# Kernel tuning notes

Measured on AMD Instinct MI355X. Metric: run time of the kernel, lower is better.

## Reference

```python
import jax, jax.numpy as jnp
import numpy as np

B, S, C, H = 8, 8192, 512, 128


def setup_inputs() -> dict:
    key = jax.random.key(0)
    k1, k2 = jax.random.split(key)
    x = jax.random.normal(k1, (B, S, C), dtype=jnp.float32)
    # nn.Linear default init: U(-1/sqrt(fan_in), 1/sqrt(fan_in))
    bound = 1.0 / np.sqrt(C)
    W = jax.random.uniform(k2, (C, H), dtype=jnp.float32, minval=-bound, maxval=bound)
    b = jnp.zeros((H,), dtype=jnp.float32)
    return {"x": x, "W": W, "b": b}


def reference(x, W, b):
    # block = identity; attn = Linear(C->H) then Softmax over sequence dim (dim=1)
    logits = jnp.einsum("bsc,ch->bsh", x, W) + b          # [B, S, H]
    a = jax.nn.softmax(logits, axis=1)                     # softmax over S
    ctx = jnp.einsum("bsh,bsc->bhc", a, x)                 # a^T @ x  -> [B, H, C]
    return jnp.einsum("bsh,bhc->bsc", a, ctx)              # a @ (a^T @ x)
```

## Files before the change

### kernel.cpp

```cpp
#include <hip/hip_runtime.h>

typedef float  f32x4 __attribute__((ext_vector_type(4)));
typedef short  s16x8 __attribute__((ext_vector_type(8)));
typedef unsigned short u16;

#define OFF_E     0ULL
#define OFF_ET    16777216ULL
#define OFF_EPART 33554432ULL
#define OFF_GT    67108864ULL
#define OFF_WT    68157440ULL
#define OFF_ZP    68288512ULL
#define OFF_RZ2   68550656ULL
#define WS_NEED   68554752ULL

#define GLL16(g, l)                                                          \
  __builtin_amdgcn_global_load_lds(                                          \
      (const __attribute__((address_space(1))) void*)(g),                    \
      (__attribute__((address_space(3))) void*)(l), 16, 0, 0)

#define KEY3(r) ((((r) >> 3) ^ ((r) << 1)) & 7)

__device__ __forceinline__ u16 f2bf(float f) {
  unsigned u = __float_as_uint(f);
  return (u16)((u + 0x8000u) >> 16);
}
__device__ __forceinline__ unsigned pack2(float a, float b) {
  unsigned ua = __float_as_uint(a), ub = __float_as_uint(b);
  return ((ua + 0x8000u) >> 16) | ((ub + 0x8000u) & 0xffff0000u);
}

__global__ __launch_bounds__(256) void k_wt(const float* __restrict__ W,
                                            u16* __restrict__ WtImg) {
  int idx = blockIdx.x * 256 + threadIdx.x;
  int h = idx & 127, c = idx >> 7;
  int kt = c >> 6, oct = (c >> 3) & 7, t = c & 7;
  WtImg[kt * 8192 + h * 64 + ((oct ^ (h & 7)) * 8) + t] = f2bf(W[c * 128 + h]);
}

__global__ __launch_bounds__(256) void k_logits_e(
    const float* __restrict__ x, const u16* __restrict__ WtImg,
    u16* __restrict__ eImg, u16* __restrict__ eTImg, float* __restrict__ zpart) {
  __shared__ __align__(16) u16 smem[4 * 8192];
  __shared__ float zs[512];
  u16* const sm = smem;
  const int tid = threadIdx.x;
  const int lane = tid & 63, wave = tid >> 6;
  const int l15 = lane & 15, quad = lane >> 4;
  const int mt = blockIdx.x;
  const int rowBase = mt << 7;
  const int q = tid & 3, rb = tid >> 2;

  f32x4 acc[2][8];
#pragma unroll
  for (int i = 0; i < 2; ++i)
#pragma unroll
    for (int j = 0; j < 8; ++j) acc[i][j] = (f32x4){0.f, 0.f, 0.f, 0.f};

  f32x4 xv[2][4];

  {
    const char* srcB = (const char*)WtImg + wave * 4096 + lane * 16;
    char* dstB = (char*)(smem + 16384) + wave * 4096;
#pragma unroll
    for (int i = 0; i < 4; ++i) GLL16(srcB + i * 1024, dstB + i * 1024);
  }
#pragma unroll
  for (int rep = 0; rep < 2; ++rep) {
    const int r = rb + rep * 64;
    const float* src = x + (size_t)(rowBase + r) * 512 + q * 4;
#pragma unroll
    for (int j = 0; j < 4; ++j) xv[rep][j] = *(const f32x4*)(src + j * 16);
  }
#pragma unroll
  for (int rep = 0; rep < 2; ++rep) {
    const int r = rb + rep * 64;
#pragma unroll
    for (int j = 0; j < 4; ++j) {
      const int chunk = (2 * j + (q >> 1)) ^ (r & 7);
      unsigned* dst = (unsigned*)&smem[r * 64 + chunk * 8 + (q & 1) * 4];
      dst[0] = pack2(xv[rep][j][0], xv[rep][j][1]);
      dst[1] = pack2(xv[rep][j][2], xv[rep][j][3]);
    }
  }
  __syncthreads();

  for (int kt = 0; kt < 8; ++kt) {
    const int cur = kt & 1;
    u16* lAc = smem + (cur ? 8192 : 0);
    u16* lBc = smem + 16384 + (cur ? 8192 : 0);
    if (kt < 7) {
      const char* srcB = (const char*)WtImg + (size_t)(kt + 1) * 16384 + wave * 4096 + lane * 16;
      char* dstB = (char*)(smem + 16384 + (cur ? 0 : 8192)) + wave * 4096;
#pragma unroll
      for (int i = 0; i < 4; ++i) GLL16(srcB + i * 1024, dstB + i * 1024);
      const int k0 = (kt + 1) << 6;
#pragma unroll
      for (int rep = 0; rep < 2; ++rep) {
        const int r = rb + rep * 64;
        const float* src = x + (size_t)(rowBase + r) * 512 + k0 + q * 4;
#pragma unroll
        for (int j = 0; j < 4; ++j) xv[rep][j] = *(const f32x4*)(src + j * 16);
      }
    }
#pragma unroll
    for (int kk = 0; kk < 2; ++kk) {
      s16x8 af[2], bf[8];
#pragma unroll
      for (int i = 0; i < 2; ++i) {
        const int r = wave * 32 + i * 16 + l15;
        af[i] = *(const s16x8*)&lAc[r * 64 + (((kk * 4 + quad) ^ (r & 7)) * 8)];
      }
#pragma unroll
      for (int j = 0; j < 8; ++j) {
        const int r = j * 16 + l15;
        bf[j] = *(const s16x8*)&lBc[r * 64 + (((kk * 4 + quad) ^ (r & 7)) * 8)];
      }
#pragma unroll
      for (int i = 0; i < 2; ++i)
#pragma unroll
        for (int j = 0; j < 8; ++j)
          acc[i][j] = __builtin_amdgcn_mfma_f32_16x16x32_bf16(af[i], bf[j], acc[i][j], 0, 0, 0);
    }
    if (kt < 7) {
      u16* lAn = smem + (cur ? 0 : 8192);
#pragma unroll
      for (int rep = 0; rep < 2; ++rep) {
        const int r = rb + rep * 64;
#pragma unroll
        for (int j = 0; j < 4; ++j) {
          const int chunk = (2 * j + (q >> 1)) ^ (r & 7);
          unsigned* dst = (unsigned*)&lAn[r * 64 + chunk * 8 + (q & 1) * 4];
          dst[0] = pack2(xv[rep][j][0], xv[rep][j][1]);
          dst[1] = pack2(xv[rep][j][2], xv[rep][j][3]);
        }
      }
    }
    __syncthreads();
  }

  float ex[2][8][4];
  float cs[8];
#pragma unroll
  for (int j = 0; j < 8; ++j) cs[j] = 0.f;
#pragma unroll
  for (int i = 0; i < 2; ++i)
#pragma unroll
    for (int j = 0; j < 8; ++j)
#pragma unroll
      for (int rr = 0; rr < 4; ++rr) {
        float l = acc[i][j][rr];
        l = fminf(fmaxf(l, -30.f), 30.f);
        float t = __expf(l);
        ex[i][j][rr] = t;
        cs[j] += t;
      }
#pragma unroll
  for (int j = 0; j < 8; ++j) {
    cs[j] += __shfl_xor(cs[j], 16);
    cs[j] += __shfl_xor(cs[j], 32);
  }
  if (quad == 0) {
#pragma unroll
    for (int j = 0; j < 8; ++j) zs[wave * 128 + j * 16 + l15] = cs[j];
  }
  __syncthreads();

#pragma unroll
  for (int i = 0; i < 2; ++i)
#pragma unroll
    for (int j = 0; j < 8; ++j)
#pragma unroll
      for (int rr = 0; rr < 4; ++rr) {
        int s = wave * 32 + i * 16 + quad * 4 + rr;
        int h = j * 16 + l15;
        sm[s * 128 + (((h >> 3) ^ (s & 15)) * 8) + (h & 7)] = f2bf(ex[i][j][rr]);
      }
  if (tid < 128)
    zpart[mt * 128 + tid] = zs[tid] + zs[128 + tid] + zs[256 + tid] + zs[384 + tid];
  __syncthreads();

  {
    char* dstT = (char*)eImg + (size_t)mt * 32768;
    const char* smB = (const char*)sm;
#pragma unroll
    for (int pass = 0; pass < 8; ++pass) {
      s16x8 v = *(const s16x8*)(smB + pass * 4096 + tid * 16);
      *(s16x8*)(dstT + pass * 4096 + tid * 16) = v;
    }
  }
  {
    int ck = tid & 15, hb = tid >> 4;
    int cH = ck >> 3, oct = ck & 7;
    u16* dstT = eTImg + (size_t)mt * 16384 + cH * 8192;
#pragma unroll
    for (int pass = 0; pass < 8; ++pass) {
      int h = hb + pass * 16;
      s16x8 v;
#pragma unroll
      for (int j = 0; j < 8; ++j) {
        int s = ck * 8 + j;
        v[j] = (short)sm[s * 128 + (((h >> 3) ^ (s & 15)) * 8) + (h & 7)];
      }
      *(s16x8*)(dstT + h * 64 + ((oct ^ KEY3(h)) * 8)) = v;
    }
  }
}

__global__ __launch_bounds__(256) void k_E(const float* __restrict__ x,
                                           const u16* __restrict__ eTImg,
                                           float* __restrict__ Epart) {
  __shared__ __align__(16) u16 smem[4 * 8192];
  const int tid = threadIdx.x;
  const int lane = tid & 63, wave = tid >> 6;
  const int l15 = lane & 15, quad = lane >> 4;
  const int nt = blockIdx.x;
  const int b = blockIdx.y;
  const int kc = blockIdx.z;
  const int cw = tid & 15, rg = tid >> 4;

  f32x4 acc[2][8];
#pragma unroll
  for (int i = 0; i < 2; ++i)
#pragma unroll
    for (int j = 0; j < 8; ++j) acc[i][j] = (f32x4){0.f, 0.f, 0.f, 0.f};

  f32x4 xv[4][2];

  {
    const char* srcB = (const char*)eTImg + ((size_t)(b * 128 + kc * 8) * 16384) +
                       wave * 4096 + lane * 16;
    char* dstB = (char*)(smem + 16384) + wave * 4096;
#pragma unroll
    for (int i = 0; i < 4; ++i) GLL16(srcB + i * 1024, dstB + i * 1024);
  }
  {
    const float* src = x + ((size_t)(b * 8192 + kc * 512 + rg * 4) * 512 + nt * 128 + cw * 8);
#pragma unroll
    for (int j = 0; j < 4; ++j) {
      xv[j][0] = *(const f32x4*)(src + (size_t)j * 512);
      xv[j][1] = *(const f32x4*)(src + (size_t)j * 512 + 4);
    }
  }
#pragma unroll
  for (int i = 0; i < 8; ++i) {
    const int cl = cw * 8 + i;
    unsigned wv[2];
    if (i < 4) {
      wv[0] = pack2(xv[0][0][i], xv[1][0][i]);
      wv[1] = pack2(xv[2][0][i], xv[3][0][i]);
    } else {
      wv[0] = pack2(xv[0][1][i - 4], xv[1][1][i - 4]);
      wv[1] = pack2(xv[2][1][i - 4], xv[3][1][i - 4]);
    }
    *(unsigned*)&smem[cl * 64 + (((rg >> 1) ^ KEY3(cl)) * 8) + (rg & 1) * 4] = wv[0];
    *(unsigned*)&smem[cl * 64 + (((rg >> 1) ^ KEY3(cl)) * 8) + (rg & 1) * 4 + 2] = wv[1];
  }
  __syncthreads();

  for (int kt = 0; kt < 8; ++kt) {
    const int cur = kt & 1;
    u16* lAc = smem + (cur ? 8192 : 0);
    u16* lBc = smem + 16384 + (cur ? 8192 : 0);
    if (kt < 7) {
      const char* srcB = (const char*)eTImg +
                         ((size_t)(b * 128 + kc * 8 + kt + 1) * 16384) +
                         wave * 4096 + lane * 16;
      char* dstB = (char*)(smem + 16384 + (cur ? 0 : 8192)) + wave * 4096;
#pragma unroll
      for (int i = 0; i < 4; ++i) GLL16(srcB + i * 1024, dstB + i * 1024);
      const float* src = x + ((size_t)(b * 8192 + kc * 512 + (kt + 1) * 64 + rg * 4) * 512 +
                              nt * 128 + cw * 8);
#pragma unroll
      for (int j = 0; j < 4; ++j) {
        xv[j][0] = *(const f32x4*)(src + (size_t)j * 512);
        xv[j][1] = *(const f32x4*)(src + (size_t)j * 512 + 4);
      }
    }
#pragma unroll
    for (int kk = 0; kk < 2; ++kk) {
      s16x8 af[2], bf[8];
#pragma unroll
      for (int i = 0; i < 2; ++i) {
        const int r = wave * 32 + i * 16 + l15;
        af[i] = *(const s16x8*)&lAc[r * 64 + (((kk * 4 + quad) ^ KEY3(r)) * 8)];
      }
#pragma unroll
      for (int j = 0; j < 8; ++j) {
        const int n = j * 16 + l15;
        bf[j] = *(const s16x8*)&lBc[n * 64 + (((kk * 4 + quad) ^ KEY3(n)) * 8)];
      }
#pragma unroll
      for (int i = 0; i < 2; ++i)
#pragma unroll
        for (int j = 0; j < 8; ++j)
          acc[i][j] = __builtin_amdgcn_mfma_f32_16x16x32_bf16(af[i], bf[j], acc[i][j], 0, 0, 0);
    }
    if (kt < 7) {
      u16* lAn = smem + (cur ? 0 : 8192);
#pragma unroll
      for (int i = 0; i < 8; ++i) {
        const int cl = cw * 8 + i;
        unsigned wv[2];
        if (i < 4) {
          wv[0] = pack2(xv[0][0][i], xv[1][0][i]);
          wv[1] = pack2(xv[2][0][i], xv[3][0][i]);
        } else {
          wv[0] = pack2(xv[0][1][i - 4], xv[1][1][i - 4]);
          wv[1] = pack2(xv[2][1][i - 4], xv[3][1][i - 4]);
        }
        *(unsigned*)&lAn[cl * 64 + (((rg >> 1) ^ KEY3(cl)) * 8) + (rg & 1) * 4] = wv[0];
        *(unsigned*)&lAn[cl * 64 + (((rg >> 1) ^ KEY3(cl)) * 8) + (rg & 1) * 4 + 2] = wv[1];
      }
    }
    __syncthreads();
  }
  float* dst = Epart + ((size_t)(kc * 8 + b) * 512 + nt * 128) * 128;
#pragma unroll
  for (int i = 0; i < 2; ++i)
#pragma unroll
    for (int j = 0; j < 8; ++j)
#pragma unroll
      for (int rr = 0; rr < 4; ++rr) {
        int c = wave * 32 + i * 16 + quad * 4 + rr;
        int h = j * 16 + l15;
        dst[(size_t)c * 128 + h] = acc[i][j][rr];
      }
}

__global__ __launch_bounds__(256) void k_G(const float* __restrict__ Epart,
                                           const float* __restrict__ zpart,
                                           u16* __restrict__ GtImg) {
  __shared__ float rzs[128];
  const int tid = threadIdx.x;
  const int bidx = blockIdx.x;
  const int b = bidx >> 5;
  if (tid < 128) {
    float z = 0.f;
#pragma unroll 8
    for (int i = 0; i < 64; ++i) z += zpart[(b * 64 + i) * 128 + tid];
    rzs[tid] = 1.0f / (z * z);
  }
  __syncthreads();
  int idx = bidx * 256 + tid;
  int h8 = idx & 15, c = (idx >> 4) & 511;
  f32x4 s0 = {0.f, 0.f, 0.f, 0.f}, s1 = {0.f, 0.f, 0.f, 0.f};
#pragma unroll
  for (int p = 0; p < 16; ++p) {
    const float* src = Epart + (((size_t)(p * 8 + b) * 512 + c) * 128 + h8 * 8);
    s0 += *(const f32x4*)src;
    s1 += *(const f32x4*)(src + 4);
  }
  f32x4 z0 = *(const f32x4*)&rzs[h8 * 8];
  f32x4 z1 = *(const f32x4*)&rzs[h8 * 8 + 4];
  unsigned ov[4];
  ov[0] = pack2(s0[0] * z0[0], s0[1] * z0[1]);
  ov[1] = pack2(s0[2] * z0[2], s0[3] * z0[3]);
  ov[2] = pack2(s1[0] * z1[0], s1[1] * z1[1]);
  ov[3] = pack2(s1[2] * z1[2], s1[3] * z1[3]);
  int r = c & 63, ct = c >> 6;
  *(s16x8*)(GtImg + ((size_t)(b * 8 + ct) * 8192) + r * 128 + ((h8 ^ (r & 15)) * 8)) =
      *(s16x8*)ov;
}

__global__ __launch_bounds__(256) void k_out(const u16* __restrict__ eImg,
                                             const u16* __restrict__ GtImg,
                                             float* __restrict__ out) {
  __shared__ __align__(16) u16 lA[128 * 128];
  __shared__ __align__(16) u16 lBd[2 * 64 * 128];
  const int tid = threadIdx.x;
  const int lane = tid & 63, wave = tid >> 6;
  const int l15 = lane & 15, quad = lane >> 4;
  const int st = blockIdx.x;
  const int b = blockIdx.y;

  {
    const char* src = (const char*)eImg + ((size_t)(b * 64 + st) * 32768) +
                      wave * 8192 + lane * 16;
    char* dst = (char*)lA + wave * 8192;
#pragma unroll
    for (int i = 0; i < 8; ++i) GLL16(src + i * 1024, dst + i * 1024);
  }
  {
    const char* src = (const char*)GtImg + ((size_t)(b * 8) * 16384) +
                      wave * 4096 + lane * 16;
    char* dst = (char*)lBd + wave * 4096;
#pragma unroll
    for (int i = 0; i < 4; ++i) GLL16(src + i * 1024, dst + i * 1024);
  }
  __syncthreads();

  for (int ct = 0; ct < 8; ++ct) {
    const int cur = ct & 1;
    u16* lBc = lBd + (cur ? 8192 : 0);
    if (ct < 7) {
      const char* src = (const char*)GtImg + ((size_t)(b * 8 + ct + 1) * 16384) +
                        wave * 4096 + lane * 16;
      char* dst = (char*)(lBd + (cur ? 0 : 8192)) + wave * 4096;
#pragma unroll
      for (int i = 0; i < 4; ++i) GLL16(src + i * 1024, dst + i * 1024);
    }
    f32x4 acc[2][4];
#pragma unroll
    for (int i = 0; i < 2; ++i)
#pragma unroll
      for (int j = 0; j < 4; ++j) acc[i][j] = (f32x4){0.f, 0.f, 0.f, 0.f};
#pragma unroll
    for (int kk = 0; kk < 4; ++kk) {
      s16x8 af[2], bf[4];
#pragma unroll
      for (int i = 0; i < 2; ++i) {
        const int r = wave * 32 + i * 16 + l15;
        af[i] = *(const s16x8*)&lA[r * 128 + (((kk * 4 + quad) ^ (r & 15)) * 8)];
      }
#pragma unroll
      for (int j = 0; j < 4; ++j) {
        const int n = j * 16 + l15;
        bf[j] = *(const s16x8*)&lBc[n * 128 + (((kk * 4 + quad) ^ (n & 15)) * 8)];
      }
#pragma unroll
      for (int i = 0; i < 2; ++i)
#pragma unroll
        for (int j = 0; j < 4; ++j)
          acc[i][j] = __builtin_amdgcn_mfma_f32_16x16x32_bf16(af[i], bf[j], acc[i][j], 0, 0, 0);
    }
#pragma unroll
    for (int i = 0; i < 2; ++i)
#pragma unroll
      for (int j = 0; j < 4; ++j)
#pragma unroll
        for (int rr = 0; rr < 4; ++rr) {
          int s = wave * 32 + i * 16 + quad * 4 + rr;
          int c = ct * 64 + j * 16 + l15;
          __builtin_nontemporal_store(
              acc[i][j][rr], &out[(size_t)(b * 8192 + st * 128 + s) * 512 + c]);
        }
    __syncthreads();
  }
}

extern "C" void kernel_launch(void* const* d_in, const int* in_sizes, int n_in,
                              void* d_out, int out_size, void* d_ws, size_t ws_size,
                              hipStream_t stream) {
  if (ws_size < (size_t)WS_NEED) return;
  const float* x = (const float*)d_in[0];
  const float* W = (const float*)d_in[1];
  float* out = (float*)d_out;
  char* ws = (char*)d_ws;
  u16* eImg = (u16*)(ws + OFF_E);
  u16* eTImg = (u16*)(ws + OFF_ET);
  float* Epart = (float*)(ws + OFF_EPART);
  u16* GtImg = (u16*)(ws + OFF_GT);
  u16* WtImg = (u16*)(ws + OFF_WT);
  float* zpart = (float*)(ws + OFF_ZP);

  k_wt<<<256, 256, 0, stream>>>(W, WtImg);
  k_logits_e<<<512, 256, 0, stream>>>(x, WtImg, eImg, eTImg, zpart);
  k_E<<<dim3(4, 8, 16), 256, 0, stream>>>(x, eTImg, Epart);
  k_G<<<256, 256, 0, stream>>>(Epart, zpart, GtImg);
  k_out<<<dim3(64, 8), 256, 0, stream>>>(eImg, GtImg, out);
}
```

Before: 301.7 us.

## Fuse five kernel launches into one persistent kernel with grid barriers

Merges the weight transpose, logits/exp, E partial GEMM, G reduction and output GEMM into a single 512-block kernel, with atomic-counter grid barriers between phases. The goal is to remove the launch gaps and tail idle time between the five separate kernels. This relies on all 512 blocks being co-resident (launch_bounds 256,2 with about 66KB of shared memory per block). The spin barriers add their own cost, and the phases keep the same block counts as before.

```diff
diff --git a/kernel.cpp b/kernel.cpp
--- a/kernel.cpp
+++ b/kernel.cpp
@@ -10,8 +10,10 @@
 #define OFF_GT    67108864ULL
 #define OFF_WT    68157440ULL
 #define OFF_ZP    68288512ULL
-#define OFF_RZ2   68550656ULL
+#define OFF_BAR   68550656ULL
 #define WS_NEED   68554752ULL
+
+#define NBLK 512u
 
 #define GLL16(g, l)                                                          \
   __builtin_amdgcn_global_load_lds(                                          \
@@ -29,247 +31,229 @@
   return ((ua + 0x8000u) >> 16) | ((ub + 0x8000u) & 0xffff0000u);
 }
 
-__global__ __launch_bounds__(256) void k_wt(const float* __restrict__ W,
-                                            u16* __restrict__ WtImg) {
-  int idx = blockIdx.x * 256 + threadIdx.x;
-  int h = idx & 127, c = idx >> 7;
-  int kt = c >> 6, oct = (c >> 3) & 7, t = c & 7;
-  WtImg[kt * 8192 + h * 64 + ((oct ^ (h & 7)) * 8) + t] = f2bf(W[c * 128 + h]);
-}
-
-__global__ __launch_bounds__(256) void k_logits_e(
-    const float* __restrict__ x, const u16* __restrict__ WtImg,
-    u16* __restrict__ eImg, u16* __restrict__ eTImg, float* __restrict__ zpart) {
-  __shared__ __align__(16) u16 smem[4 * 8192];
-  __shared__ float zs[512];
-  u16* const sm = smem;
+__device__ __forceinline__ void gbar(unsigned* cnt) {
+  __syncthreads();
+  if (threadIdx.x == 0) {
+    __threadfence();
+    atomicAdd(cnt, 1u);
+    while (atomicAdd(cnt, 0u) < NBLK) __builtin_amdgcn_s_sleep(2);
+    __threadfence();
+  }
+  __syncthreads();
+}
+
+__global__ void k_init(unsigned* bar) {
+  if (threadIdx.x < 8) bar[threadIdx.x] = 0u;
+}
+
+__global__ __launch_bounds__(256, 2) void k_fused(
+    const float* __restrict__ x, const float* __restrict__ W,
+    float* __restrict__ out, u16* __restrict__ eImg, u16* __restrict__ eTImg,
+    float* __restrict__ Epart, u16* __restrict__ GtImg, u16* __restrict__ WtImg,
+    float* __restrict__ zpart, unsigned* bar) {
+  __shared__ __align__(16) char SMEM[67584];
   const int tid = threadIdx.x;
+  const int bid = blockIdx.x;
   const int lane = tid & 63, wave = tid >> 6;
   const int l15 = lane & 15, quad = lane >> 4;
-  const int mt = blockIdx.x;
-  const int rowBase = mt << 7;
-  const int q = tid & 3, rb = tid >> 2;
-
-  f32x4 acc[2][8];
-#pragma unroll
-  for (int i = 0; i < 2; ++i)
-#pragma unroll
-    for (int j = 0; j < 8; ++j) acc[i][j] = (f32x4){0.f, 0.f, 0.f, 0.f};
-
-  f32x4 xv[2][4];
+
+  if (tid < 128) {
+    int idx = bid * 128 + tid;
+    int h = idx & 127, c = idx >> 7;
+    int kt = c >> 6, oct = (c >> 3) & 7, t = c & 7;
+    WtImg[kt * 8192 + h * 64 + ((oct ^ (h & 7)) * 8) + t] = f2bf(W[c * 128 + h]);
+  }
+  gbar(bar + 0);
 
   {
-    const char* srcB = (const char*)WtImg + wave * 4096 + lane * 16;
-    char* dstB = (char*)(smem + 16384) + wave * 4096;
-#pragma unroll
-    for (int i = 0; i < 4; ++i) GLL16(srcB + i * 1024, dstB + i * 1024);
-  }
-#pragma unroll
-  for (int rep = 0; rep < 2; ++rep) {
-    const int r = rb + rep * 64;
-    const float* src = x + (size_t)(rowBase + r) * 512 + q * 4;
-#pragma unroll
-    for (int j = 0; j < 4; ++j) xv[rep][j] = *(const f32x4*)(src + j * 16);
-  }
-#pragma unroll
-  for (int rep = 0; rep < 2; ++rep) {
-    const int r = rb + rep * 64;
-#pragma unroll
-    for (int j = 0; j < 4; ++j) {
-      const int chunk = (2 * j + (q >> 1)) ^ (r & 7);
-      unsigned* dst = (unsigned*)&smem[r * 64 + chunk * 8 + (q & 1) * 4];
-      dst[0] = pack2(xv[rep][j][0], xv[rep][j][1]);
-      dst[1] = pack2(xv[rep][j][2], xv[rep][j][3]);
-    }
-  }
-  __syncthreads();
-
-  for (int kt = 0; kt < 8; ++kt) {
-    const int cur = kt & 1;
-    u16* lAc = smem + (cur ? 8192 : 0);
-    u16* lBc = smem + 16384 + (cur ? 8192 : 0);
-    if (kt < 7) {
-      const char* srcB = (const char*)WtImg + (size_t)(kt + 1) * 16384 + wave * 4096 + lane * 16;
-      char* dstB = (char*)(smem + 16384 + (cur ? 0 : 8192)) + wave * 4096;
+    u16* smem = (u16*)SMEM;
+    float* zs = (float*)(SMEM + 65536);
+    u16* const sm = smem;
+    const int mt = bid;
+    const int rowBase = mt << 7;
+    const int q = tid & 3, rb = tid >> 2;
+
+    f32x4 acc[2][8];
+#pragma unroll
+    for (int i = 0; i < 2; ++i)
+#pragma unroll
+      for (int j = 0; j < 8; ++j) acc[i][j] = (f32x4){0.f, 0.f, 0.f, 0.f};
+
+    f32x4 xv[2][4];
+
+    {
+      const char* srcB = (const char*)WtImg + wave * 4096 + lane * 16;
+      char* dstB = (char*)(smem + 16384) + wave * 4096;
 #pragma unroll
       for (int i = 0; i < 4; ++i) GLL16(srcB + i * 1024, dstB + i * 1024);
-      const int k0 = (kt + 1) << 6;
-#pragma unroll
-      for (int rep = 0; rep < 2; ++rep) {
-        const int r = rb + rep * 64;
-        const float* src = x + (size_t)(rowBase + r) * 512 + k0 + q * 4;
-#pragma unroll
-        for (int j = 0; j < 4; ++j) xv[rep][j] = *(const f32x4*)(src + j * 16);
-      }
-    }
-#pragma unroll
-    for (int kk = 0; kk < 2; ++kk) {
-      s16x8 af[2], bf[8];
-#pragma unroll
-      for (int i = 0; i < 2; ++i) {
-        const int r = wave * 32 + i * 16 + l15;
-        af[i] = *(const s16x8*)&lAc[r * 64 + (((kk * 4 + quad) ^ (r & 7)) * 8)];
-      }
-#pragma unroll
-      for (int j = 0; j < 8; ++j) {
-        const int r = j * 16 + l15;
-        bf[j] = *(const s16x8*)&lBc[r * 64 + (((kk * 4 + quad) ^ (r & 7)) * 8)];
-      }
-#pragma unroll
-      for (int i = 0; i < 2; ++i)
-#pragma unroll
-        for (int j = 0; j < 8; ++j)
-          acc[i][j] = __builtin_amdgcn_mfma_f32_16x16x32_bf16(af[i], bf[j], acc[i][j], 0, 0, 0);
-    }
-    if (kt < 7) {
-      u16* lAn = smem + (cur ? 0 : 8192);
-#pragma unroll
-      for (int rep = 0; rep < 2; ++rep) {
-        const int r = rb + rep * 64;
-#pragma unroll
-        for (int j = 0; j < 4; ++j) {
-          const int chunk = (2 * j + (q >> 1)) ^ (r & 7);
-          unsigned* dst = (unsigned*)&lAn[r * 64 + chunk * 8 + (q & 1) * 4];
-          dst[0] = pack2(xv[rep][j][0], xv[rep][j][1]);
-          dst[1] = pack2(xv[rep][j][2], xv[rep][j][3]);
-        }
-      }
-    }
-    __syncthreads();
-  }
-
-  float ex[2][8][4];
-  float cs[8];
-#pragma unroll
-  for (int j = 0; j < 8; ++j) cs[j] = 0.f;
-#pragma unroll
-  for (int i = 0; i < 2; ++i)
-#pragma unroll
-    for (int j = 0; j < 8; ++j)
-#pragma unroll
-      for (int rr = 0; rr < 4; ++rr) {
-        float l = acc[i][j][rr];
-        l = fminf(fmaxf(l, -30.f), 30.f);
-        float t = __expf(l);
-        ex[i][j][rr] = t;
-        cs[j] += t;
-      }
-#pragma unroll
-  for (int j = 0; j < 8; ++j) {
-    cs[j] += __shfl_xor(cs[j], 16);
-    cs[j] += __shfl_xor(cs[j], 32);
-  }
-  if (quad == 0) {
-#pragma unroll
-    for (int j = 0; j < 8; ++j) zs[wave * 128 + j * 16 + l15] = cs[j];
-  }
-  __syncthreads();
-
-#pragma unroll
-  for (int i = 0; i < 2; ++i)
-#pragma unroll
-    for (int j = 0; j < 8; ++j)
-#pragma unroll
-      for (int rr = 0; rr < 4; ++rr) {
-        int s = wave * 32 + i * 16 + quad * 4 + rr;
-        int h = j * 16 + l15;
-        sm[s * 128 + (((h >> 3) ^ (s & 15)) * 8) + (h & 7)] = f2bf(ex[i][j][rr]);
-      }
-  if (tid < 128)
-    zpart[mt * 128 + tid] = zs[tid] + zs[128 + tid] + zs[256 + tid] + zs[384 + tid];
-  __syncthreads();
+    }
+#pragma unroll
+    for (int rep = 0; rep < 2; ++rep) {
+      const int r = rb + rep * 64;
+      const float* src = x + (size_t)(rowBase + r) * 512 + q * 4;
+#pragma unroll
+      for (int j = 0; j < 4; ++j) xv[rep][j] = *(const f32x4*)(src + j * 16);
+    }
+#pragma unroll
+    for (int rep = 0; rep < 2; ++rep) {
+      const int r = rb + rep * 64;
+#pragma unroll
+      for (int j = 0; j < 4; ++j) {
+        const int chunk = (2 * j + (q >> 1)) ^ (r & 7);
+        unsigned* dst = (unsigned*)&smem[r * 64 + chunk * 8 + (q & 1) * 4];
+        dst[0] = pack2(xv[rep][j][0], xv[rep][j][1]);
+        dst[1] = pack2(xv[rep][j][2], xv[rep][j][3]);
+      }
+    }
+    __syncthreads();
+
+    for (int kt = 0; kt < 8; ++kt) {
+      const int cur = kt & 1;
+      u16* lAc = smem + (cur ? 8192 : 0);
+      u16* lBc = smem + 16384 + (cur ? 8192 : 0);
+      if (kt < 7) {
+        const char* srcB = (const char*)WtImg + (size_t)(kt + 1) * 16384 + wave * 4096 + lane * 16;
+        char* dstB = (char*)(smem + 16384 + (cur ? 0 : 8192)) + wave * 4096;
+#pragma unroll
+        for (int i = 0; i < 4; ++i) GLL16(srcB + i * 1024, dstB + i * 1024);
+        const int k0 = (kt + 1) << 6;
+#pragma unroll
+        for (int rep = 0; rep < 2; ++rep) {
+          const int r = rb + rep * 64;
+          const float* src = x + (size_t)(rowBase + r) * 512 + k0 + q * 4;
+#pragma unroll
+          for (int j = 0; j < 4; ++j) xv[rep][j] = *(const f32x4*)(src + j * 16);
+        }
+      }
+#pragma unroll
+      for (int kk = 0; kk < 2; ++kk) {
+        s16x8 af[2], bf[8];
+#pragma unroll
+        for (int i = 0; i < 2; ++i) {
+          const int r = wave * 32 + i * 16 + l15;
+          af[i] = *(const s16x8*)&lAc[r * 64 + (((kk * 4 + quad) ^ (r & 7)) * 8)];
+        }
+#pragma unroll
+        for (int j = 0; j < 8; ++j) {
+          const int r = j * 16 + l15;
+          bf[j] = *(const s16x8*)&lBc[r * 64 + (((kk * 4 + quad) ^ (r & 7)) * 8)];
+        }
+#pragma unroll
+        for (int i = 0; i < 2; ++i)
+#pragma unroll
+          for (int j = 0; j < 8; ++j)
+            acc[i][j] = __builtin_amdgcn_mfma_f32_16x16x32_bf16(af[i], bf[j], acc[i][j], 0, 0, 0);
+      }
+      if (kt < 7) {
+        u16* lAn = smem + (cur ? 0 : 8192);
+#pragma unroll
+        for (int rep = 0; rep < 2; ++rep) {
+          const int r = rb + rep * 64;
+#pragma unroll
+          for (int j = 0; j < 4; ++j) {
+            const int chunk = (2 * j + (q >> 1)) ^ (r & 7);
+            unsigned* dst = (unsigned*)&lAn[r * 64 + chunk * 8 + (q & 1) * 4];
+            dst[0] = pack2(xv[rep][j][0], xv[rep][j][1]);
+            dst[1] = pack2(xv[rep][j][2], xv[rep][j][3]);
+          }
+        }
+      }
+      __syncthreads();
+    }
+
+    float ex[2][8][4];
+    float cs[8];
+#pragma unroll
+    for (int j = 0; j < 8; ++j) cs[j] = 0.f;
+#pragma unroll
+    for (int i = 0; i < 2; ++i)
+#pragma unroll
+      for (int j = 0; j < 8; ++j)
+#pragma unroll
+        for (int rr = 0; rr < 4; ++rr) {
+          float l = acc[i][j][rr];
+          l = fminf(fmaxf(l, -30.f), 30.f);
+          float t = __expf(l);
+          ex[i][j][rr] = t;
+          cs[j] += t;
+        }
+#pragma unroll
+    for (int j = 0; j < 8; ++j) {
+      cs[j] += __shfl_xor(cs[j], 16);
+      cs[j] += __shfl_xor(cs[j], 32);
+    }
+    if (quad == 0) {
+#pragma unroll
+      for (int j = 0; j < 8; ++j) zs[wave * 128 + j * 16 + l15] = cs[j];
+    }
+    __syncthreads();
+
+#pragma unroll
+    for (int i = 0; i < 2; ++i)
+#pragma unroll
+      for (int j = 0; j < 8; ++j)
+#pragma unroll
+        for (int rr = 0; rr < 4; ++rr) {
+          int s = wave * 32 + i * 16 + quad * 4 + rr;
+          int h = j * 16 + l15;
+          sm[s * 128 + (((h >> 3) ^ (s & 15)) * 8) + (h & 7)] = f2bf(ex[i][j][rr]);
+        }
+    if (tid < 128)
+      zpart[mt * 128 + tid] = zs[tid] + zs[128 + tid] + zs[256 + tid] + zs[384 + tid];
+    __syncthreads();
+
+    {
+      char* dstT = (char*)eImg + (size_t)mt * 32768;
+      const char* smB = (const char*)sm;
+#pragma unroll
+      for (int pass = 0; pass < 8; ++pass) {
+        s16x8 v = *(const s16x8*)(smB + pass * 4096 + tid * 16);
+        *(s16x8*)(dstT + pass * 4096 + tid * 16) = v;
+      }
+    }
+    {
+      int ck = tid & 15, hb = tid >> 4;
+      int cH = ck >> 3, oct = ck & 7;
+      u16* dstT = eTImg + (size_t)mt * 16384 + cH * 8192;
+#pragma unroll
+      for (int pass = 0; pass < 8; ++pass) {
+        int h = hb + pass * 16;
+        s16x8 v;
+#pragma unroll
+        for (int j = 0; j < 8; ++j) {
+          int s = ck * 8 + j;
+          v[j] = (short)sm[s * 128 + (((h >> 3) ^ (s & 15)) * 8) + (h & 7)];
+        }
+        *(s16x8*)(dstT + h * 64 + ((oct ^ KEY3(h)) * 8)) = v;
+      }
+    }
+  }
+  gbar(bar + 1);
 
   {
-    char* dstT = (char*)eImg + (size_t)mt * 32768;
-    const char* smB = (const char*)sm;
-#pragma unroll
-    for (int pass = 0; pass < 8; ++pass) {
-      s16x8 v = *(const s16x8*)(smB + pass * 4096 + tid * 16);
-      *(s16x8*)(dstT + pass * 4096 + tid * 16) = v;
-    }
-  }
-  {
-    int ck = tid & 15, hb = tid >> 4;
-    int cH = ck >> 3, oct = ck & 7;
-    u16* dstT = eTImg + (size_t)mt * 16384 + cH * 8192;
-#pragma unroll
-    for (int pass = 0; pass < 8; ++pass) {
-      int h = hb + pass * 16;
-      s16x8 v;
-#pragma unroll
-      for (int j = 0; j < 8; ++j) {
-        int s = ck * 8 + j;
-        v[j] = (short)sm[s * 128 + (((h >> 3) ^ (s & 15)) * 8) + (h & 7)];
-      }
-      *(s16x8*)(dstT + h * 64 + ((oct ^ KEY3(h)) * 8)) = v;
-    }
-  }
-}
-
-__global__ __launch_bounds__(256) void k_E(const float* __restrict__ x,
-                                           const u16* __restrict__ eTImg,
-                                           float* __restrict__ Epart) {
-  __shared__ __align__(16) u16 smem[4 * 8192];
-  const int tid = threadIdx.x;
-  const int lane = tid & 63, wave = tid >> 6;
-  const int l15 = lane & 15, quad = lane >> 4;
-  const int nt = blockIdx.x;
-  const int b = blockIdx.y;
-  const int kc = blockIdx.z;
-  const int cw = tid & 15, rg = tid >> 4;
-
-  f32x4 acc[2][8];
-#pragma unroll
-  for (int i = 0; i < 2; ++i)
-#pragma unroll
-    for (int j = 0; j < 8; ++j) acc[i][j] = (f32x4){0.f, 0.f, 0.f, 0.f};
-
-  f32x4 xv[4][2];
-
-  {
-    const char* srcB = (const char*)eTImg + ((size_t)(b * 128 + kc * 8) * 16384) +
-                       wave * 4096 + lane * 16;
-    char* dstB = (char*)(smem + 16384) + wave * 4096;
-#pragma unroll
-    for (int i = 0; i < 4; ++i) GLL16(srcB + i * 1024, dstB + i * 1024);
-  }
-  {
-    const float* src = x + ((size_t)(b * 8192 + kc * 512 + rg * 4) * 512 + nt * 128 + cw * 8);
-#pragma unroll
-    for (int j = 0; j < 4; ++j) {
-      xv[j][0] = *(const f32x4*)(src + (size_t)j * 512);
-      xv[j][1] = *(const f32x4*)(src + (size_t)j * 512 + 4);
-    }
-  }
-#pragma unroll
-  for (int i = 0; i < 8; ++i) {
-    const int cl = cw * 8 + i;
-    unsigned wv[2];
-    if (i < 4) {
-      wv[0] = pack2(xv[0][0][i], xv[1][0][i]);
-      wv[1] = pack2(xv[2][0][i], xv[3][0][i]);
-    } else {
-      wv[0] = pack2(xv[0][1][i - 4], xv[1][1][i - 4]);
-      wv[1] = pack2(xv[2][1][i - 4], xv[3][1][i - 4]);
-    }
-    *(unsigned*)&smem[cl * 64 + (((rg >> 1) ^ KEY3(cl)) * 8) + (rg & 1) * 4] = wv[0];
-    *(unsigned*)&smem[cl * 64 + (((rg >> 1) ^ KEY3(cl)) * 8) + (rg & 1) * 4 + 2] = wv[1];
-  }
-  __syncthreads();
-
-  for (int kt = 0; kt < 8; ++kt) {
-    const int cur = kt & 1;
-    u16* lAc = smem + (cur ? 8192 : 0);
-    u16* lBc = smem + 16384 + (cur ? 8192 : 0);
-    if (kt < 7) {
-      const char* srcB = (const char*)eTImg +
-                         ((size_t)(b * 128 + kc * 8 + kt + 1) * 16384) +
+    u16* smem = (u16*)SMEM;
+    const int nt = bid & 3;
+    const int b = (bid >> 2) & 7;
+    const int kc = bid >> 5;
+    const int cw = tid & 15, rg = tid >> 4;
+
+    f32x4 acc[2][8];
+#pragma unroll
+    for (int i = 0; i < 2; ++i)
+#pragma unroll
+      for (int j = 0; j < 8; ++j) acc[i][j] = (f32x4){0.f, 0.f, 0.f, 0.f};
+
+    f32x4 xv[4][2];
+
+    {
+      const char* srcB = (const char*)eTImg + ((size_t)(b * 128 + kc * 8) * 16384) +
                          wave * 4096 + lane * 16;
-      char* dstB = (char*)(smem + 16384 + (cur ? 0 : 8192)) + wave * 4096;
+      char* dstB = (char*)(smem + 16384) + wave * 4096;
 #pragma unroll
       for (int i = 0; i < 4; ++i) GLL16(srcB + i * 1024, dstB + i * 1024);
-      const float* src = x + ((size_t)(b * 8192 + kc * 512 + (kt + 1) * 64 + rg * 4) * 512 +
-                              nt * 128 + cw * 8);
+    }
+    {
+      const float* src = x + ((size_t)(b * 8192 + kc * 512 + rg * 4) * 512 + nt * 128 + cw * 8);
 #pragma unroll
       for (int j = 0; j < 4; ++j) {
         xv[j][0] = *(const f32x4*)(src + (size_t)j * 512);
@@ -277,164 +261,193 @@
       }
     }
 #pragma unroll
-    for (int kk = 0; kk < 2; ++kk) {
-      s16x8 af[2], bf[8];
-#pragma unroll
-      for (int i = 0; i < 2; ++i) {
-        const int r = wave * 32 + i * 16 + l15;
-        af[i] = *(const s16x8*)&lAc[r * 64 + (((kk * 4 + quad) ^ KEY3(r)) * 8)];
-      }
-#pragma unroll
-      for (int j = 0; j < 8; ++j) {
-        const int n = j * 16 + l15;
-        bf[j] = *(const s16x8*)&lBc[n * 64 + (((kk * 4 + quad) ^ KEY3(n)) * 8)];
-      }
+    for (int i = 0; i < 8; ++i) {
+      const int cl = cw * 8 + i;
+      unsigned wv[2];
+      if (i < 4) {
+        wv[0] = pack2(xv[0][0][i], xv[1][0][i]);
+        wv[1] = pack2(xv[2][0][i], xv[3][0][i]);
+      } else {
+        wv[0] = pack2(xv[0][1][i - 4], xv[1][1][i - 4]);
+        wv[1] = pack2(xv[2][1][i - 4], xv[3][1][i - 4]);
+      }
+      *(unsigned*)&smem[cl * 64 + (((rg >> 1) ^ KEY3(cl)) * 8) + (rg & 1) * 4] = wv[0];
+      *(unsigned*)&smem[cl * 64 + (((rg >> 1) ^ KEY3(cl)) * 8) + (rg & 1) * 4 + 2] = wv[1];
+    }
+    __syncthreads();
+
+    for (int kt = 0; kt < 8; ++kt) {
+      const int cur = kt & 1;
+      u16* lAc = smem + (cur ? 8192 : 0);
+      u16* lBc = smem + 16384 + (cur ? 8192 : 0);
+      if (kt < 7) {
+        const char* srcB = (const char*)eTImg +
+                           ((size_t)(b * 128 + kc * 8 + kt + 1) * 16384) +
+                           wave * 4096 + lane * 16;
+        char* dstB = (char*)(smem + 16384 + (cur ? 0 : 8192)) + wave * 4096;
+#pragma unroll
+        for (int i = 0; i < 4; ++i) GLL16(srcB + i * 1024, dstB + i * 1024);
+        const float* src = x + ((size_t)(b * 8192 + kc * 512 + (kt + 1) * 64 + rg * 4) * 512 +
+                                nt * 128 + cw * 8);
+#pragma unroll
+        for (int j = 0; j < 4; ++j) {
+          xv[j][0] = *(const f32x4*)(src + (size_t)j * 512);
+          xv[j][1] = *(const f32x4*)(src + (size_t)j * 512 + 4);
+        }
+      }
+#pragma unroll
+      for (int kk = 0; kk < 2; ++kk) {
+        s16x8 af[2], bf[8];
+#pragma unroll
+        for (int i = 0; i < 2; ++i) {
+          const int r = wave * 32 + i * 16 + l15;
+          af[i] = *(const s16x8*)&lAc[r * 64 + (((kk * 4 + quad) ^ KEY3(r)) * 8)];
+        }
+#pragma unroll
+        for (int j = 0; j < 8; ++j) {
+          const int n = j * 16 + l15;
+          bf[j] = *(const s16x8*)&lBc[n * 64 + (((kk * 4 + quad) ^ KEY3(n)) * 8)];
+        }
+#pragma unroll
+        for (int i = 0; i < 2; ++i)
+#pragma unroll
+          for (int j = 0; j < 8; ++j)
+            acc[i][j] = __builtin_amdgcn_mfma_f32_16x16x32_bf16(af[i], bf[j], acc[i][j], 0, 0, 0);
+      }
+      if (kt < 7) {
+        u16* lAn = smem + (cur ? 0 : 8192);
+#pragma unroll
+        for (int i = 0; i < 8; ++i) {
+          const int cl = cw * 8 + i;
+          unsigned wv[2];
+          if (i < 4) {
+            wv[0] = pack2(xv[0][0][i], xv[1][0][i]);
+            wv[1] = pack2(xv[2][0][i], xv[3][0][i]);
+          } else {
+            wv[0] = pack2(xv[0][1][i - 4], xv[1][1][i - 4]);
+            wv[1] = pack2(xv[2][1][i - 4], xv[3][1][i - 4]);
+          }
+          *(unsigned*)&lAn[cl * 64 + (((rg >> 1) ^ KEY3(cl)) * 8) + (rg & 1) * 4] = wv[0];
+          *(unsigned*)&lAn[cl * 64 + (((rg >> 1) ^ KEY3(cl)) * 8) + (rg & 1) * 4 + 2] = wv[1];
+        }
+      }
+      __syncthreads();
+    }
+    float* dst = Epart + ((size_t)(kc * 8 + b) * 512 + nt * 128) * 128;
+#pragma unroll
+    for (int i = 0; i < 2; ++i)
+#pragma unroll
+      for (int j = 0; j < 8; ++j)
+#pragma unroll
+        for (int rr = 0; rr < 4; ++rr) {
+          int c = wave * 32 + i * 16 + quad * 4 + rr;
+          int h = j * 16 + l15;
+          dst[(size_t)c * 128 + h] = acc[i][j][rr];
+        }
+  }
+  gbar(bar + 2);
+
+  if (bid < 256) {
+    float* rzs = (float*)SMEM;
+    const int b = bid >> 5;
+    if (tid < 128) {
+      float z = 0.f;
+#pragma unroll 8
+      for (int i = 0; i < 64; ++i) z += zpart[(b * 64 + i) * 128 + tid];
+      rzs[tid] = 1.0f / (z * z);
+    }
+    __syncthreads();
+    int idx = bid * 256 + tid;
+    int h8 = idx & 15, c = (idx >> 4) & 511;
+    f32x4 s0 = {0.f, 0.f, 0.f, 0.f}, s1 = {0.f, 0.f, 0.f, 0.f};
+#pragma unroll
+    for (int p = 0; p < 16; ++p) {
+      const float* src = Epart + (((size_t)(p * 8 + b) * 512 + c) * 128 + h8 * 8);
+      s0 += *(const f32x4*)src;
+      s1 += *(const f32x4*)(src + 4);
+    }
+    f32x4 z0 = *(const f32x4*)&rzs[h8 * 8];
+    f32x4 z1 = *(const f32x4*)&rzs[h8 * 8 + 4];
+    unsigned ov[4];
+    ov[0] = pack2(s0[0] * z0[0], s0[1] * z0[1]);
+    ov[1] = pack2(s0[2] * z0[2], s0[3] * z0[3]);
+    ov[2] = pack2(s1[0] * z1[0], s1[1] * z1[1]);
+    ov[3] = pack2(s1[2] * z1[2], s1[3] * z1[3]);
+    int r = c & 63, ct = c >> 6;
+    *(s16x8*)(GtImg + ((size_t)(b * 8 + ct) * 8192) + r * 128 + ((h8 ^ (r & 15)) * 8)) =
+        *(s16x8*)ov;
+  }
+  gbar(bar + 3);
+
+  {
+    u16* lA = (u16*)SMEM;
+    u16* lBd = (u16*)(SMEM + 32768);
+    const int st = bid & 63;
+    const int b = bid >> 6;
+
+    {
+      const char* src = (const char*)eImg + ((size_t)(b * 64 + st) * 32768) +
+                        wave * 8192 + lane * 16;
+      char* dst = (char*)lA + wave * 8192;
+#pragma unroll
+      for (int i = 0; i < 8; ++i) GLL16(src + i * 1024, dst + i * 1024);
+    }
+    {
+      const char* src = (const char*)GtImg + ((size_t)(b * 8) * 16384) +
+                        wave * 4096 + lane * 16;
+      char* dst = (char*)lBd + wave * 4096;
+#pragma unroll
+      for (int i = 0; i < 4; ++i) GLL16(src + i * 1024, dst + i * 1024);
+    }
+    __syncthreads();
+
+    for (int ct = 0; ct < 8; ++ct) {
+      const int cur = ct & 1;
+      u16* lBc = lBd + (cur ? 8192 : 0);
+      if (ct < 7) {
+        const char* src = (const char*)GtImg + ((size_t)(b * 8 + ct + 1) * 16384) +
+                          wave * 4096 + lane * 16;
+        char* dst = (char*)(lBd + (cur ? 0 : 8192)) + wave * 4096;
+#pragma unroll
+        for (int i = 0; i < 4; ++i) GLL16(src + i * 1024, dst + i * 1024);
+      }
+      f32x4 acc[2][4];
 #pragma unroll
       for (int i = 0; i < 2; ++i)
 #pragma unroll
-        for (int j = 0; j < 8; ++j)
-          acc[i][j] = __builtin_amdgcn_mfma_f32_16x16x32_bf16(af[i], bf[j], acc[i][j], 0, 0, 0);
-    }
-    if (kt < 7) {
-      u16* lAn = smem + (cur ? 0 : 8192);
-#pragma unroll
-      for (int i = 0; i < 8; ++i) {
-        const int cl = cw * 8 + i;
-        unsigned wv[2];
-        if (i < 4) {
-          wv[0] = pack2(xv[0][0][i], xv[1][0][i]);
-          wv[1] = pack2(xv[2][0][i], xv[3][0][i]);
-        } else {
-          wv[0] = pack2(xv[0][1][i - 4], xv[1][1][i - 4]);
-          wv[1] = pack2(xv[2][1][i - 4], xv[3][1][i - 4]);
-        }
-        *(unsigned*)&lAn[cl * 64 + (((rg >> 1) ^ KEY3(cl)) * 8) + (rg & 1) * 4] = wv[0];
-        *(unsigned*)&lAn[cl * 64 + (((rg >> 1) ^ KEY3(cl)) * 8) + (rg & 1) * 4 + 2] = wv[1];
-      }
-    }
-    __syncthreads();
-  }
-  float* dst = Epart + ((size_t)(kc * 8 + b) * 512 + nt * 128) * 128;
-#pragma unroll
-  for (int i = 0; i < 2; ++i)
-#pragma unroll
-    for (int j = 0; j < 8; ++j)
-#pragma unroll
-      for (int rr = 0; rr < 4; ++rr) {
-        int c = wave * 32 + i * 16 + quad * 4 + rr;
-        int h = j * 16 + l15;
-        dst[(size_t)c * 128 + h] = acc[i][j][rr];
-      }
-}
-
-__global__ __launch_bounds__(256) void k_G(const float* __restrict__ Epart,
-                                           const float* __restrict__ zpart,
-                                           u16* __restrict__ GtImg) {
-  __shared__ float rzs[128];
-  const int tid = threadIdx.x;
-  const int bidx = blockIdx.x;
-  const int b = bidx >> 5;
-  if (tid < 128) {
-    float z = 0.f;
-#pragma unroll 8
-    for (int i = 0; i < 64; ++i) z += zpart[(b * 64 + i) * 128 + tid];
-    rzs[tid] = 1.0f / (z * z);
-  }
-  __syncthreads();
-  int idx = bidx * 256 + tid;
-  int h8 = idx & 15, c = (idx >> 4) & 511;
-  f32x4 s0 = {0.f, 0.f, 0.f, 0.f}, s1 = {0.f, 0.f, 0.f, 0.f};
-#pragma unroll
-  for (int p = 0; p < 16; ++p) {
-    const float* src = Epart + (((size_t)(p * 8 + b) * 512 + c) * 128 + h8 * 8);
-    s0 += *(const f32x4*)src;
-    s1 += *(const f32x4*)(src + 4);
-  }
-  f32x4 z0 = *(const f32x4*)&rzs[h8 * 8];
-  f32x4 z1 = *(const f32x4*)&rzs[h8 * 8 + 4];
-  unsigned ov[4];
-  ov[0] = pack2(s0[0] * z0[0], s0[1] * z0[1]);
-  ov[1] = pack2(s0[2] * z0[2], s0[3] * z0[3]);
-  ov[2] = pack2(s1[0] * z1[0], s1[1] * z1[1]);
-  ov[3] = pack2(s1[2] * z1[2], s1[3] * z1[3]);
-  int r = c & 63, ct = c >> 6;
-  *(s16x8*)(GtImg + ((size_t)(b * 8 + ct) * 8192) + r * 128 + ((h8 ^ (r & 15)) * 8)) =
-      *(s16x8*)ov;
-}
-
-__global__ __launch_bounds__(256) void k_out(const u16* __restrict__ eImg,
-                                             const u16* __restrict__ GtImg,
-                                             float* __restrict__ out) {
-  __shared__ __align__(16) u16 lA[128 * 128];
-  __shared__ __align__(16) u16 lBd[2 * 64 * 128];
-  const int tid = threadIdx.x;
-  const int lane = tid & 63, wave = tid >> 6;
-  const int l15 = lane & 15, quad = lane >> 4;
-  const int st = blockIdx.x;
-  const int b = blockIdx.y;
-
-  {
-    const char* src = (const char*)eImg + ((size_t)(b * 64 + st) * 32768) +
-                      wave * 8192 + lane * 16;
-    char* dst = (char*)lA + wave * 8192;
-#pragma unroll
-    for (int i = 0; i < 8; ++i) GLL16(src + i * 1024, dst + i * 1024);
-  }
-  {
-    const char* src = (const char*)GtImg + ((size_t)(b * 8) * 16384) +
-                      wave * 4096 + lane * 16;
-    char* dst = (char*)lBd + wave * 4096;
-#pragma unroll
-    for (int i = 0; i < 4; ++i) GLL16(src + i * 1024, dst + i * 1024);
-  }
-  __syncthreads();
-
-  for (int ct = 0; ct < 8; ++ct) {
-    const int cur = ct & 1;
-    u16* lBc = lBd + (cur ? 8192 : 0);
-    if (ct < 7) {
-      const char* src = (const char*)GtImg + ((size_t)(b * 8 + ct + 1) * 16384) +
-                        wave * 4096 + lane * 16;
-      char* dst = (char*)(lBd + (cur ? 0 : 8192)) + wave * 4096;
-#pragma unroll
-      for (int i = 0; i < 4; ++i) GLL16(src + i * 1024, dst + i * 1024);
-    }
-    f32x4 acc[2][4];
-#pragma unroll
-    for (int i = 0; i < 2; ++i)
-#pragma unroll
-      for (int j = 0; j < 4; ++j) acc[i][j] = (f32x4){0.f, 0.f, 0.f, 0.f};
-#pragma unroll
-    for (int kk = 0; kk < 4; ++kk) {
-      s16x8 af[2], bf[4];
-#pragma unroll
-      for (int i = 0; i < 2; ++i) {
-        const int r = wave * 32 + i * 16 + l15;
-        af[i] = *(const s16x8*)&lA[r * 128 + (((kk * 4 + quad) ^ (r & 15)) * 8)];
-      }
-#pragma unroll
-      for (int j = 0; j < 4; ++j) {
-        const int n = j * 16 + l15;
-        bf[j] = *(const s16x8*)&lBc[n * 128 + (((kk * 4 + quad) ^ (n & 15)) * 8)];
+        for (int j = 0; j < 4; ++j) acc[i][j] = (f32x4){0.f, 0.f, 0.f, 0.f};
+#pragma unroll
+      for (int kk = 0; kk < 4; ++kk) {
+        s16x8 af[2], bf[4];
+#pragma unroll
+        for (int i = 0; i < 2; ++i) {
+          const int r = wave * 32 + i * 16 + l15;
+          af[i] = *(const s16x8*)&lA[r * 128 + (((kk * 4 + quad) ^ (r & 15)) * 8)];
+        }
+#pragma unroll
+        for (int j = 0; j < 4; ++j) {
+          const int n = j * 16 + l15;
+          bf[j] = *(const s16x8*)&lBc[n * 128 + (((kk * 4 + quad) ^ (n & 15)) * 8)];
+        }
+#pragma unroll
+        for (int i = 0; i < 2; ++i)
+#pragma unroll
+          for (int j = 0; j < 4; ++j)
+            acc[i][j] = __builtin_amdgcn_mfma_f32_16x16x32_bf16(af[i], bf[j], acc[i][j], 0, 0, 0);
       }
 #pragma unroll
       for (int i = 0; i < 2; ++i)
 #pragma unroll
         for (int j = 0; j < 4; ++j)
-          acc[i][j] = __builtin_amdgcn_mfma_f32_16x16x32_bf16(af[i], bf[j], acc[i][j], 0, 0, 0);
-    }
-#pragma unroll
-    for (int i = 0; i < 2; ++i)
-#pragma unroll
-      for (int j = 0; j < 4; ++j)
-#pragma unroll
-        for (int rr = 0; rr < 4; ++rr) {
-          int s = wave * 32 + i * 16 + quad * 4 + rr;
-          int c = ct * 64 + j * 16 + l15;
-          __builtin_nontemporal_store(
-              acc[i][j][rr], &out[(size_t)(b * 8192 + st * 128 + s) * 512 + c]);
-        }
-    __syncthreads();
+#pragma unroll
+          for (int rr = 0; rr < 4; ++rr) {
+            int s = wave * 32 + i * 16 + quad * 4 + rr;
+            int c = ct * 64 + j * 16 + l15;
+            __builtin_nontemporal_store(
+                acc[i][j][rr], &out[(size_t)(b * 8192 + st * 128 + s) * 512 + c]);
+          }
+      __syncthreads();
+    }
   }
 }
 
@@ -452,10 +465,9 @@
   u16* GtImg = (u16*)(ws + OFF_GT);
   u16* WtImg = (u16*)(ws + OFF_WT);
   float* zpart = (float*)(ws + OFF_ZP);
-
-  k_wt<<<256, 256, 0, stream>>>(W, WtImg);
-  k_logits_e<<<512, 256, 0, stream>>>(x, WtImg, eImg, eTImg, zpart);
-  k_E<<<dim3(4, 8, 16), 256, 0, stream>>>(x, eTImg, Epart);
-  k_G<<<256, 256, 0, stream>>>(Epart, zpart, GtImg);
-  k_out<<<dim3(64, 8), 256, 0, stream>>>(eImg, GtImg, out);
-}
+  unsigned* bar = (unsigned*)(ws + OFF_BAR);
+
+  k_init<<<1, 64, 0, stream>>>(bar);
+  k_fused<<<NBLK, 256, 0, stream>>>(x, W, out, eImg, eTImg, Epart, GtImg, WtImg,
+                                    zpart, bar);
+}
```

Result: slower. 518.2 us (+71.8%).
